# Kernel optimization log

Hardware: AMD Instinct MI355X
Metric: run time of the kernel (lower is better)

The kernel has to match this reference:

```python
import jax, jax.numpy as jnp
import numpy as np

NUM_LAYERS = 24
LN_EPS = 1e-5


def setup_inputs() -> dict:
    key = jax.random.key(0)
    ks = jax.random.split(key, 8)
    B, S = 256, 8192
    x = jax.random.uniform(ks[0], (B, S, 5), dtype=jnp.float32)
    # per-layer LayerNorm(4) params (torch default init: weight=1, bias=0; use
    # randomized values so the gather is non-trivial)
    ln_w = 1.0 + 0.1 * jax.random.normal(ks[1], (NUM_LAYERS, 4), dtype=jnp.float32)
    ln_b = 0.1 * jax.random.normal(ks[2], (NUM_LAYERS, 4), dtype=jnp.float32)
    # MLP 5 -> 64 -> 32 -> 1 (dropout inactive in eval mode)
    W1 = jax.random.normal(ks[3], (64, 5), dtype=jnp.float32) / np.sqrt(5)
    b1 = jnp.zeros((64,), dtype=jnp.float32)
    W2 = jax.random.normal(ks[4], (32, 64), dtype=jnp.float32) / np.sqrt(64)
    b2 = jnp.zeros((32,), dtype=jnp.float32)
    W3 = jax.random.normal(ks[5], (1, 32), dtype=jnp.float32) / np.sqrt(32)
    b3 = jnp.zeros((1,), dtype=jnp.float32)
    return {"x": x, "ln_w": ln_w, "ln_b": ln_b, "W1": W1, "b1": b1,
            "W2": W2, "b2": b2, "W3": W3, "b3": b3}


def reference(x, ln_w, ln_b, W1, b1, W2, b2, W3, b3):
    B, S, _ = x.shape
    x_flat = x.reshape(-1, 5)                      # [N, 5]
    layer_pos = x_flat[:, -1]                      # [N]
    layer_ids = jnp.clip((layer_pos * NUM_LAYERS).astype(jnp.int32), 0, NUM_LAYERS - 1)
    feats = x_flat[:, :4]                          # [N, 4]
    # vectorized per-token LayerNorm: gather per-token gamma/beta by layer id
    mean = jnp.mean(feats, axis=-1, keepdims=True)
    var = jnp.mean(jnp.square(feats - mean), axis=-1, keepdims=True)  # biased, as torch LN
    normed = (feats - mean) * jax.lax.rsqrt(var + LN_EPS)
    normed = normed * ln_w[layer_ids] + ln_b[layer_ids]               # [N, 4]
    x_norm = jnp.concatenate([normed, layer_pos[:, None]], axis=1)    # [N, 5]
    h = jax.nn.relu(x_norm @ W1.T + b1)            # [N, 64]
    h = jax.nn.relu(h @ W2.T + b2)                 # [N, 32]
    scores = h @ W3.T + b3                         # [N, 1]
    return scores.reshape(B, S)
```

## Files before the change

kernel.cpp:

```cpp
#include <hip/hip_runtime.h>
#include <hip/hip_bf16.h>
#include <stdint.h>

#define NUM_LAYERS 24
#define LN_EPS 1e-5f
#define N_ROWS (256 * 8192)
#define ROWS_PER_ITER 64
#define NUM_ITERS (N_ROWS / ROWS_PER_ITER)
#define NUM_BLOCKS 2048

typedef __attribute__((ext_vector_type(4)))  uint32_t u32x4;
typedef __attribute__((ext_vector_type(16))) float    f32x16;
typedef __attribute__((ext_vector_type(2)))  float    f32x2;
typedef __attribute__((ext_vector_type(2)))  __fp16   h16x2;

__device__ __forceinline__ uint32_t pk_f16_rtz(float lo, float hi) {
    h16x2 v = __builtin_amdgcn_cvt_pkrtz(lo, hi);
    uint32_t u; __builtin_memcpy(&u, &v, 4);
    return u;
}
__device__ __forceinline__ uint32_t pk_f16_rne(float lo, float hi) {
    __fp16 a = (__fp16)lo, b = (__fp16)hi;
    uint16_t ua, ub;
    __builtin_memcpy(&ua, &a, 2); __builtin_memcpy(&ub, &b, 2);
    return (uint32_t)ua | ((uint32_t)ub << 16);
}
__device__ __forceinline__ uint32_t pk_relu_f16(uint32_t d) {
    h16x2 v; __builtin_memcpy(&v, &d, 4);
    h16x2 z = {(__fp16)0.0f, (__fp16)0.0f};
    v = __builtin_elementwise_max(v, z);
    uint32_t u; __builtin_memcpy(&u, &v, 4);
    return u;
}

__device__ __forceinline__ u32x4 make_frag(uint32_t d0, uint32_t d1,
                                           uint32_t d2, uint32_t d3) {
    u32x4 f; f.x = d0; f.y = d1; f.z = d2; f.w = d3;
    return f;
}

__device__ __forceinline__ f32x16 mfma_f16_c(u32x4 a, u32x4 b, const f32x16& c) {
    f32x16 d;
    asm("s_nop 2\n\tv_mfma_f32_32x32x16_f16 %0, %1, %2, %3"
        : "=&v"(d) : "v"(a), "v"(b), "v"(c));
    return d;
}
__device__ __forceinline__ void mfma_f16_acc(f32x16& c, u32x4 a, u32x4 b) {
    asm("s_nop 2\n\tv_mfma_f32_32x32x16_f16 %0, %1, %2, %0"
        : "+v"(c) : "v"(a), "v"(b));
}
__device__ __forceinline__ void mfma_fence(f32x16& c) {
    asm volatile("s_nop 7\n\ts_nop 7\n\ts_nop 7" : "+v"(c));
}
__device__ __forceinline__ void mfma_fence2(f32x16& c0, f32x16& c1) {
    asm volatile("s_nop 7\n\ts_nop 7\n\ts_nop 7" : "+v"(c0), "+v"(c1));
}

__device__ __forceinline__ int sigma_k(int p) {
    int hh = (p >> 2) & 1;
    int base = (p & 31) - 4 * hh;
    int r = (base & 3) + 4 * (base >> 3);
    return 32 * (p >> 5) + 16 * (r >> 3) + 8 * hh + (r & 7);
}

__global__ __launch_bounds__(256, 3) void router_mfma(
    const float* __restrict__ x,
    const float* __restrict__ ln_w,
    const float* __restrict__ ln_b,
    const float* __restrict__ W1,
    const float* __restrict__ b1,
    const float* __restrict__ W2,
    const float* __restrict__ b2,
    const float* __restrict__ W3,
    const float* __restrict__ b3,
    float* __restrict__ out)
{
    __shared__ float s_ln[NUM_LAYERS * 8];
    const int t = threadIdx.x;
    if (t < NUM_LAYERS * 4) {
        int lid = t >> 2, c = t & 3;
        s_ln[lid * 8 + c]     = ln_w[t];
        s_ln[lid * 8 + 4 + c] = ln_b[t];
    }
    __syncthreads();

    const int lane = t & 63;
    const int wid  = t >> 6;
    const int n32  = lane & 31;
    const int h    = lane >> 5;

    u32x4 a1f[2];
#pragma unroll
    for (int mt = 0; mt < 2; ++mt) {
        int p = mt * 32 + n32;
        int k = sigma_k(p);
        uint32_t d0 = pk_f16_rne(W1[k * 5 + 0], W1[k * 5 + 1]);
        uint32_t d1 = pk_f16_rne(W1[k * 5 + 2], W1[k * 5 + 3]);
        uint32_t d2 = pk_f16_rne(W1[k * 5 + 4], b1[k]);
        if (h) { d0 = 0; d1 = 0; d2 = 0; }
        a1f[mt] = make_frag(d0, d1, d2, 0);
    }

    u32x4 w2f[4];
#pragma unroll
    for (int kt = 0; kt < 4; ++kt) {
        const float* wp = W2 + n32 * 64 + kt * 16 + h * 8;
        const float4 lo = *(const float4*)(wp);
        const float4 hi = *(const float4*)(wp + 4);
        w2f[kt] = make_frag(pk_f16_rne(lo.x, lo.y), pk_f16_rne(lo.z, lo.w),
                            pk_f16_rne(hi.x, hi.y), pk_f16_rne(hi.z, hi.w));
    }

    f32x16 c2init;
    f32x2 w3p[8];
#pragma unroll
    for (int r2 = 0; r2 < 8; ++r2) {
        const int n = ((2 * r2) & 3) + 8 * (r2 >> 1) + 4 * h;
        w3p[r2] = f32x2{W3[n], W3[n + 1]};
        c2init[2 * r2]     = b2[n];
        c2init[2 * r2 + 1] = b2[n + 1];
    }
    const float b3v = b3[0];

    f32x16 zf;
#pragma unroll
    for (int i = 0; i < 16; ++i) zf[i] = 0.0f;
    const f32x2 z2 = {0.0f, 0.0f};

    const int total_waves = NUM_BLOCKS * 4;
    const int w = blockIdx.x * 4 + wid;

    int it = w;
    const float* xp0 = x + (size_t)(it * ROWS_PER_ITER + lane) * 5;
    float f0 = xp0[0], f1 = xp0[1], f2 = xp0[2], f3 = xp0[3], lp = xp0[4];

    while (true) {
        const int nit = it + total_waves;
        const bool more = nit < NUM_ITERS;
        const float* nxp =
            x + (size_t)((more ? nit : it) * ROWS_PER_ITER + lane) * 5;
        const float nf0 = nxp[0], nf1 = nxp[1], nf2 = nxp[2], nf3 = nxp[3],
                    nlp = nxp[4];

        const int rowBase = it * ROWS_PER_ITER;

        int lid = (int)(lp * (float)NUM_LAYERS);
        lid = lid < 0 ? 0 : (lid > NUM_LAYERS - 1 ? NUM_LAYERS - 1 : lid);

        const float m  = (f0 + f1 + f2 + f3) * 0.25f;
        const float d0 = f0 - m, d1 = f1 - m, d2 = f2 - m, d3 = f3 - m;
        const float var = (d0 * d0 + d1 * d1 + d2 * d2 + d3 * d3) * 0.25f;
        const float r   = rsqrtf(var + LN_EPS);

        const float4 g  = *(const float4*)(s_ln + lid * 8);
        const float4 bb = *(const float4*)(s_ln + lid * 8 + 4);

        const float xn0 = fmaf(d0 * r, g.x, bb.x);
        const float xn1 = fmaf(d1 * r, g.y, bb.y);
        const float xn2 = fmaf(d2 * r, g.z, bb.z);
        const float xn3 = fmaf(d3 * r, g.w, bb.w);

        const uint32_t e0 = pk_f16_rtz(xn0, xn1);
        const uint32_t e1 = pk_f16_rtz(xn2, xn3);
        const uint32_t e2 = pk_f16_rtz(lp, 1.0f);
        const uint32_t x0 = __shfl_xor((int)e0, 32, 64);
        const uint32_t x1 = __shfl_xor((int)e1, 32, 64);
        const uint32_t x2 = __shfl_xor((int)e2, 32, 64);

        const u32x4 bf_t0 = make_frag(e0, e1, e2, 0u);
        const u32x4 bf_t1 = make_frag(x0, x1, x2, 0u);

        float res[2];
#pragma unroll
        for (int tile = 0; tile < 2; ++tile) {
            const u32x4 b1f = tile ? bf_t1 : bf_t0;

            f32x16 c1a = mfma_f16_c(a1f[0], b1f, zf);
            f32x16 c1b = mfma_f16_c(a1f[1], b1f, zf);
            mfma_fence2(c1a, c1b);

            u32x4 h1f[4];
#pragma unroll
            for (int kt = 0; kt < 4; ++kt) {
                const f32x16& c1 = (kt < 2) ? c1a : c1b;
                const int roff = 8 * (kt & 1);
                uint32_t dw[4];
#pragma unroll
                for (int d = 0; d < 4; ++d)
                    dw[d] = pk_relu_f16(
                        pk_f16_rtz(c1[roff + 2 * d], c1[roff + 2 * d + 1]));
                h1f[kt] = make_frag(dw[0], dw[1], dw[2], dw[3]);
            }

            f32x16 c2 = mfma_f16_c(w2f[0], h1f[0], c2init);
#pragma unroll
            for (int kt = 1; kt < 4; ++kt)
                mfma_f16_acc(c2, w2f[kt], h1f[kt]);
            mfma_fence(c2);

            f32x2 acc = z2;
#pragma unroll
            for (int r2 = 0; r2 < 8; ++r2) {
                f32x2 v = {c2[2 * r2], c2[2 * r2 + 1]};
                v = __builtin_elementwise_max(v, z2);
                acc = v * w3p[r2] + acc;
            }
            float part = acc.x + acc.y;
            part += __shfl_xor(part, 32, 64);
            res[tile] = part;
        }

        out[rowBase + lane] = (h ? res[1] : res[0]) + b3v;

        if (!more) break;
        it = nit;
        f0 = nf0; f1 = nf1; f2 = nf2; f3 = nf3; lp = nlp;
    }
}

extern "C" void kernel_launch(void* const* d_in, const int* in_sizes, int n_in,
                              void* d_out, int out_size, void* d_ws, size_t ws_size,
                              hipStream_t stream) {
    const float* x    = (const float*)d_in[0];
    const float* ln_w = (const float*)d_in[1];
    const float* ln_b = (const float*)d_in[2];
    const float* W1   = (const float*)d_in[3];
    const float* b1   = (const float*)d_in[4];
    const float* W2   = (const float*)d_in[5];
    const float* b2   = (const float*)d_in[6];
    const float* W3   = (const float*)d_in[7];
    const float* b3   = (const float*)d_in[8];
    float* out = (float*)d_out;

    router_mfma<<<NUM_BLOCKS, 256, 0, stream>>>(x, ln_w, ln_b, W1, b1, W2, b2,
                                                W3, b3, out);
}
```

Before: 109.5 us.

## Process 32 rows per wave iteration, dropping cross-half shuffles and duplicating loads

Each wave now handles 32 rows per iteration instead of 64. Both half-waves load the same row, so the three shuffles that swapped packed inputs between halves are gone and each iteration runs one tile instead of two. The MFMA calls are grouped into multi-instruction asm blocks using an inline zero accumulator. The LayerNorm parameter table is transposed in shared memory, the grid size is doubled and the occupancy hint is raised. In exchange, half the lanes compute redundant input work, global loads of x are duplicated across the two halves, and only half the lanes store results.

```diff
diff --git a/kernel.cpp b/kernel.cpp
--- a/kernel.cpp
+++ b/kernel.cpp
@@ -1,13 +1,12 @@
 #include <hip/hip_runtime.h>
-#include <hip/hip_bf16.h>
 #include <stdint.h>
 
 #define NUM_LAYERS 24
 #define LN_EPS 1e-5f
 #define N_ROWS (256 * 8192)
-#define ROWS_PER_ITER 64
+#define ROWS_PER_ITER 32
 #define NUM_ITERS (N_ROWS / ROWS_PER_ITER)
-#define NUM_BLOCKS 2048
+#define NUM_BLOCKS 4096
 
 typedef __attribute__((ext_vector_type(4)))  uint32_t u32x4;
 typedef __attribute__((ext_vector_type(16))) float    f32x16;
@@ -39,18 +38,31 @@
     return f;
 }
 
-__device__ __forceinline__ f32x16 mfma_f16_c(u32x4 a, u32x4 b, const f32x16& c) {
-    f32x16 d;
-    asm("s_nop 2\n\tv_mfma_f32_32x32x16_f16 %0, %1, %2, %3"
-        : "=&v"(d) : "v"(a), "v"(b), "v"(c));
-    return d;
-}
-__device__ __forceinline__ void mfma_f16_acc(f32x16& c, u32x4 a, u32x4 b) {
-    asm("s_nop 2\n\tv_mfma_f32_32x32x16_f16 %0, %1, %2, %0"
-        : "+v"(c) : "v"(a), "v"(b));
-}
-__device__ __forceinline__ void mfma_fence(f32x16& c) {
-    asm volatile("s_nop 7\n\ts_nop 7\n\ts_nop 7" : "+v"(c));
+__device__ __forceinline__ void mfma_l1(f32x16& d0, f32x16& d1,
+                                        const u32x4& a0, const u32x4& a1,
+                                        const u32x4& b) {
+    asm("s_nop 2\n\t"
+        "v_mfma_f32_32x32x16_f16 %0, %2, %4, 0\n\t"
+        "v_mfma_f32_32x32x16_f16 %1, %3, %4, 0"
+        : "=&v"(d0), "=&v"(d1)
+        : "v"(a0), "v"(a1), "v"(b));
+}
+__device__ __forceinline__ void mfma_l2(f32x16& c, const f32x16& cinit,
+                                        const u32x4& w0, const u32x4& w1,
+                                        const u32x4& w2, const u32x4& w3,
+                                        const u32x4& h0, const u32x4& h1,
+                                        const u32x4& h2, const u32x4& h3) {
+    asm("s_nop 2\n\t"
+        "v_mfma_f32_32x32x16_f16 %0, %2, %6, %1\n\t"
+        "v_mfma_f32_32x32x16_f16 %0, %3, %7, %0\n\t"
+        "v_mfma_f32_32x32x16_f16 %0, %4, %8, %0\n\t"
+        "v_mfma_f32_32x32x16_f16 %0, %5, %9, %0"
+        : "=&v"(c)
+        : "v"(cinit), "v"(w0), "v"(w1), "v"(w2), "v"(w3),
+          "v"(h0), "v"(h1), "v"(h2), "v"(h3));
+}
+__device__ __forceinline__ void mfma_fence1(f32x16& c0) {
+    asm volatile("s_nop 7\n\ts_nop 7\n\ts_nop 7" : "+v"(c0));
 }
 __device__ __forceinline__ void mfma_fence2(f32x16& c0, f32x16& c1) {
     asm volatile("s_nop 7\n\ts_nop 7\n\ts_nop 7" : "+v"(c0), "+v"(c1));
@@ -63,7 +75,7 @@
     return 32 * (p >> 5) + 16 * (r >> 3) + 8 * hh + (r & 7);
 }
 
-__global__ __launch_bounds__(256, 3) void router_mfma(
+__global__ __launch_bounds__(256, 4) void router_mfma(
     const float* __restrict__ x,
     const float* __restrict__ ln_w,
     const float* __restrict__ ln_b,
@@ -75,12 +87,13 @@
     const float* __restrict__ b3,
     float* __restrict__ out)
 {
-    __shared__ float s_ln[NUM_LAYERS * 8];
+    __shared__ float s_ln[8 * NUM_LAYERS];
+
     const int t = threadIdx.x;
-    if (t < NUM_LAYERS * 4) {
-        int lid = t >> 2, c = t & 3;
-        s_ln[lid * 8 + c]     = ln_w[t];
-        s_ln[lid * 8 + 4 + c] = ln_b[t];
+    if (t < 8 * NUM_LAYERS) {
+        const int q = t & 7, lid = t >> 3;
+        s_ln[q * NUM_LAYERS + lid] =
+            (q < 4) ? ln_w[lid * 4 + q] : ln_b[lid * 4 + (q - 4)];
     }
     __syncthreads();
 
@@ -121,100 +134,80 @@
         c2init[2 * r2 + 1] = b2[n + 1];
     }
     const float b3v = b3[0];
-
-    f32x16 zf;
-#pragma unroll
-    for (int i = 0; i < 16; ++i) zf[i] = 0.0f;
     const f32x2 z2 = {0.0f, 0.0f};
 
     const int total_waves = NUM_BLOCKS * 4;
     const int w = blockIdx.x * 4 + wid;
 
     int it = w;
-    const float* xp0 = x + (size_t)(it * ROWS_PER_ITER + lane) * 5;
-    float f0 = xp0[0], f1 = xp0[1], f2 = xp0[2], f3 = xp0[3], lp = xp0[4];
+    const float* xp = x + (size_t)(it * ROWS_PER_ITER + n32) * 5;
+    float4 v4 = *(const float4*)xp;
+    float  v1 = xp[4];
+    float cf0 = v4.x, cf1 = v4.y, cf2 = v4.z, cf3 = v4.w, clp = v1;
 
     while (true) {
         const int nit = it + total_waves;
         const bool more = nit < NUM_ITERS;
         const float* nxp =
-            x + (size_t)((more ? nit : it) * ROWS_PER_ITER + lane) * 5;
-        const float nf0 = nxp[0], nf1 = nxp[1], nf2 = nxp[2], nf3 = nxp[3],
-                    nlp = nxp[4];
+            x + (size_t)((more ? nit : it) * ROWS_PER_ITER + n32) * 5;
+        const float4 nv4 = *(const float4*)nxp;
+        const float  nlp = nxp[4];
 
         const int rowBase = it * ROWS_PER_ITER;
 
-        int lid = (int)(lp * (float)NUM_LAYERS);
+        int lid = (int)(clp * (float)NUM_LAYERS);
         lid = lid < 0 ? 0 : (lid > NUM_LAYERS - 1 ? NUM_LAYERS - 1 : lid);
 
-        const float m  = (f0 + f1 + f2 + f3) * 0.25f;
-        const float d0 = f0 - m, d1 = f1 - m, d2 = f2 - m, d3 = f3 - m;
+        const float m  = (cf0 + cf1 + cf2 + cf3) * 0.25f;
+        const float d0 = cf0 - m, d1 = cf1 - m, d2 = cf2 - m, d3 = cf3 - m;
         const float var = (d0 * d0 + d1 * d1 + d2 * d2 + d3 * d3) * 0.25f;
         const float r   = rsqrtf(var + LN_EPS);
 
-        const float4 g  = *(const float4*)(s_ln + lid * 8);
-        const float4 bb = *(const float4*)(s_ln + lid * 8 + 4);
-
-        const float xn0 = fmaf(d0 * r, g.x, bb.x);
-        const float xn1 = fmaf(d1 * r, g.y, bb.y);
-        const float xn2 = fmaf(d2 * r, g.z, bb.z);
-        const float xn3 = fmaf(d3 * r, g.w, bb.w);
-
-        const uint32_t e0 = pk_f16_rtz(xn0, xn1);
-        const uint32_t e1 = pk_f16_rtz(xn2, xn3);
-        const uint32_t e2 = pk_f16_rtz(lp, 1.0f);
-        const uint32_t x0 = __shfl_xor((int)e0, 32, 64);
-        const uint32_t x1 = __shfl_xor((int)e1, 32, 64);
-        const uint32_t x2 = __shfl_xor((int)e2, 32, 64);
-
-        const u32x4 bf_t0 = make_frag(e0, e1, e2, 0u);
-        const u32x4 bf_t1 = make_frag(x0, x1, x2, 0u);
-
-        float res[2];
-#pragma unroll
-        for (int tile = 0; tile < 2; ++tile) {
-            const u32x4 b1f = tile ? bf_t1 : bf_t0;
-
-            f32x16 c1a = mfma_f16_c(a1f[0], b1f, zf);
-            f32x16 c1b = mfma_f16_c(a1f[1], b1f, zf);
-            mfma_fence2(c1a, c1b);
-
-            u32x4 h1f[4];
-#pragma unroll
-            for (int kt = 0; kt < 4; ++kt) {
-                const f32x16& c1 = (kt < 2) ? c1a : c1b;
-                const int roff = 8 * (kt & 1);
-                uint32_t dw[4];
-#pragma unroll
-                for (int d = 0; d < 4; ++d)
-                    dw[d] = pk_relu_f16(
-                        pk_f16_rtz(c1[roff + 2 * d], c1[roff + 2 * d + 1]));
-                h1f[kt] = make_frag(dw[0], dw[1], dw[2], dw[3]);
-            }
-
-            f32x16 c2 = mfma_f16_c(w2f[0], h1f[0], c2init);
-#pragma unroll
-            for (int kt = 1; kt < 4; ++kt)
-                mfma_f16_acc(c2, w2f[kt], h1f[kt]);
-            mfma_fence(c2);
-
-            f32x2 acc = z2;
-#pragma unroll
-            for (int r2 = 0; r2 < 8; ++r2) {
-                f32x2 v = {c2[2 * r2], c2[2 * r2 + 1]};
-                v = __builtin_elementwise_max(v, z2);
-                acc = v * w3p[r2] + acc;
-            }
-            float part = acc.x + acc.y;
-            part += __shfl_xor(part, 32, 64);
-            res[tile] = part;
+        const float xn0 = fmaf(d0, r * s_ln[0 * 24 + lid], s_ln[4 * 24 + lid]);
+        const float xn1 = fmaf(d1, r * s_ln[1 * 24 + lid], s_ln[5 * 24 + lid]);
+        const float xn2 = fmaf(d2, r * s_ln[2 * 24 + lid], s_ln[6 * 24 + lid]);
+        const float xn3 = fmaf(d3, r * s_ln[3 * 24 + lid], s_ln[7 * 24 + lid]);
+
+        const u32x4 b1f = make_frag(pk_f16_rtz(xn0, xn1),
+                                    pk_f16_rtz(xn2, xn3),
+                                    pk_f16_rtz(clp, 1.0f), 0u);
+
+        f32x16 c1a, c1b;
+        mfma_l1(c1a, c1b, a1f[0], a1f[1], b1f);
+        mfma_fence2(c1a, c1b);
+
+        u32x4 h1f[4];
+#pragma unroll
+        for (int kt = 0; kt < 4; ++kt) {
+            const f32x16& c1 = (kt < 2) ? c1a : c1b;
+            const int roff = 8 * (kt & 1);
+            uint32_t dw[4];
+#pragma unroll
+            for (int d = 0; d < 4; ++d)
+                dw[d] = pk_relu_f16(
+                    pk_f16_rtz(c1[roff + 2 * d], c1[roff + 2 * d + 1]));
+            h1f[kt] = make_frag(dw[0], dw[1], dw[2], dw[3]);
         }
 
-        out[rowBase + lane] = (h ? res[1] : res[0]) + b3v;
+        f32x16 c2;
+        mfma_l2(c2, c2init, w2f[0], w2f[1], w2f[2], w2f[3],
+                h1f[0], h1f[1], h1f[2], h1f[3]);
+        mfma_fence1(c2);
+
+        f32x2 acc = z2;
+#pragma unroll
+        for (int r2 = 0; r2 < 8; ++r2) {
+            f32x2 v = {c2[2 * r2], c2[2 * r2 + 1]};
+            v = __builtin_elementwise_max(v, z2);
+            acc = v * w3p[r2] + acc;
+        }
+        float part = acc.x + acc.y;
+        part += __shfl_xor(part, 32, 64);
+        if (!h) out[rowBase + n32] = part + b3v;
 
         if (!more) break;
         it = nit;
-        f0 = nf0; f1 = nf1; f2 = nf2; f3 = nf3; lp = nlp;
+        cf0 = nv4.x; cf1 = nv4.y; cf2 = nv4.z; cf3 = nv4.w; clp = nlp;
     }
 }
 
```

After: 119.3 us. +8.9%, slower.
